# Optimization experiments

Hardware: AMD Instinct MI355X
Metric: run time of the kernel (lower is better)

The kernel has to match this reference:

```python
import jax, jax.numpy as jnp
import numpy as np

DIM = 4096
HID = DIM // 4
CAPACITY = 0.5
TEMPERATURE = 1.0


def setup_inputs() -> dict:
    key = jax.random.key(0)
    k_x, k_w1, k_w2 = jax.random.split(key, 3)
    B, S = 4, 4096
    x = jax.random.normal(k_x, (B, S, DIM), dtype=jnp.float32)
    # Linear params (kaiming-ish scale)
    w1 = jax.random.normal(k_w1, (DIM, HID), dtype=jnp.float32) * (1.0 / np.sqrt(DIM))
    b1 = jnp.zeros((HID,), dtype=jnp.float32)
    w2 = jax.random.normal(k_w2, (HID, 1), dtype=jnp.float32) * (1.0 / np.sqrt(HID))
    b2 = jnp.zeros((1,), dtype=jnp.float32)
    return {"x": x, "w1": w1, "b1": b1, "w2": w2, "b2": b2}


def reference(x, w1, b1, w2, b2):
    B, S, _ = x.shape
    # tiny MLP scorer: dim -> dim//4 -> 1
    h = jax.nn.relu(jnp.einsum('bsd,dh->bsh', x, w1) + b1)
    scores = (jnp.einsum('bsh,ho->bso', h, w2) + b2)[..., 0] / TEMPERATURE  # [B, S]
    k = int(S * CAPACITY)
    topk_scores, topk_idx = jax.lax.top_k(scores, k)  # [B, k]
    rows = jnp.arange(B)[:, None]
    mask = jnp.zeros((B, S), dtype=jnp.bool_).at[rows, topk_idx].set(True)
    # torch: routing_weights[mask] = softmax(topk_scores).flatten()
    # mask-indexed assignment writes to positions in ascending index order,
    # while values stay in topk (descending-score) order -> replicate exactly.
    sorted_idx = jnp.sort(topk_idx, axis=-1)  # [B, k], ascending positions
    soft = jax.nn.softmax(topk_scores, axis=-1)  # [B, k], topk order
    routing_weights = jnp.zeros((B, S), dtype=scores.dtype).at[rows, sorted_idx].set(soft)
    return mask, routing_weights
```

## Files before the change

### kernel.cpp

```cpp
#include <hip/hip_runtime.h>
#include <math.h>

typedef _Float16 f16;
typedef _Float16 f16x8 __attribute__((ext_vector_type(8)));
typedef float    f32x4 __attribute__((ext_vector_type(4)));

#define DIMK 4096
#define HIDN 1024
#define NTOK 16384
#define SLEN 4096
#define NBATCH 4
#define KSEL 2048
#define NPART 16

#define LO_SCALE 2048.0f
#define INV_ACC_SCALE (1.0f/4194304.0f)

__device__ __forceinline__ void load_lds16(const void* g, void* l) {
    __builtin_amdgcn_global_load_lds(
        (const __attribute__((address_space(1))) unsigned int*)g,
        (__attribute__((address_space(3))) unsigned int*)l, 16, 0, 0);
}
__device__ __forceinline__ int swzf(int row) { return ((row >> 1) & 3) << 4; }

__device__ __forceinline__ void split_w(float v, f16& hi_s, f16& lo_s) {
    const f16 h = (f16)v;
    const float hf = (float)h;
    hi_s = (f16)(hf * LO_SCALE);
    lo_s = (f16)((v - hf) * LO_SCALE);
}

__device__ __forceinline__ void split8(const float4 v0, const float4 v1,
                                       f16x8& h8, f16x8& l8) {
    const float s0 = v0.x * LO_SCALE, s1 = v0.y * LO_SCALE;
    const float s2 = v0.z * LO_SCALE, s3 = v0.w * LO_SCALE;
    const float s4 = v1.x * LO_SCALE, s5 = v1.y * LO_SCALE;
    const float s6 = v1.z * LO_SCALE, s7 = v1.w * LO_SCALE;
    const auto h01 = __builtin_amdgcn_cvt_pkrtz(s0, s1);
    const auto h23 = __builtin_amdgcn_cvt_pkrtz(s2, s3);
    const auto h45 = __builtin_amdgcn_cvt_pkrtz(s4, s5);
    const auto h67 = __builtin_amdgcn_cvt_pkrtz(s6, s7);
    const auto l01 = __builtin_amdgcn_cvt_pkrtz(s0 - (float)h01[0], s1 - (float)h01[1]);
    const auto l23 = __builtin_amdgcn_cvt_pkrtz(s2 - (float)h23[0], s3 - (float)h23[1]);
    const auto l45 = __builtin_amdgcn_cvt_pkrtz(s4 - (float)h45[0], s5 - (float)h45[1]);
    const auto l67 = __builtin_amdgcn_cvt_pkrtz(s6 - (float)h67[0], s7 - (float)h67[1]);
    h8 = f16x8{(f16)h01[0], (f16)h01[1], (f16)h23[0], (f16)h23[1],
               (f16)h45[0], (f16)h45[1], (f16)h67[0], (f16)h67[1]};
    l8 = f16x8{(f16)l01[0], (f16)l01[1], (f16)l23[0], (f16)l23[1],
               (f16)l45[0], (f16)l45[1], (f16)l67[0], (f16)l67[1]};
}

__device__ __forceinline__ f32x4 mfma16(f16x8 a, f16x8 b, f32x4 c) {
    return __builtin_amdgcn_mfma_f32_16x16x32_f16(a, b, c, 0, 0, 0);
}

__global__ __launch_bounds__(256) void conv_w1_kernel(
    const float* w1, f16* wthi, f16* wtlo)
{
    __shared__ float t[64][65];
    const int bx = blockIdx.x & 15;
    const int by = blockIdx.x >> 4;
    #pragma unroll
    for (int i = 0; i < 16; ++i) {
        const int e = threadIdx.x + i * 256;
        const int r = e >> 6, c = e & 63;
        t[r][c] = w1[(size_t)(by * 64 + r) * HIDN + bx * 64 + c];
    }
    __syncthreads();
    #pragma unroll
    for (int i = 0; i < 16; ++i) {
        const int e = threadIdx.x + i * 256;
        const int nrow = e >> 6, kcol = e & 63;
        f16 h, l;
        split_w(t[kcol][nrow], h, l);
        const size_t o = (size_t)(bx * 64 + nrow) * DIMK + by * 64 + kcol;
        wthi[o] = h;
        wtlo[o] = l;
    }
}

#define TBM 256
#define TBN 256
#define TBK 32
#define BUF_BYTES 65536

__global__ __launch_bounds__(512, 2) void mod_mfma256_kernel(
    const float* x, const f16* wthi, const f16* wtlo,
    const float* b1, const float* w2, float* partials)
{
    __shared__ __align__(16) char lds[2 * BUF_BYTES];

    const int tid  = threadIdx.x;
    const int lane = tid & 63;
    const int wid  = tid >> 6;
    const int wr   = wid >> 2;
    const int wc   = wid & 3;

    const int bid  = blockIdx.x;
    const int v    = (bid & 7) * 32 + (bid >> 3);
    const int nblk = v & 3;
    const int mblk = v >> 2;
    const int tokBase = mblk * TBM;
    const int nBase   = nblk * TBN;

    int arow[2], akqq[2], adst[2];
    #pragma unroll
    for (int i = 0; i < 2; ++i) {
        const int p = tid + i * 512;
        arow[i] = p >> 2;
        akqq[i] = p & 3;
        adst[i] = arow[i] * 64 + ((akqq[i] ^ ((arow[i] >> 1) & 3)) << 4);
    }
    const f16* bsrcm[4];
    int bsrcoff[4], bdst[4];
    #pragma unroll
    for (int j = 0; j < 4; ++j) {
        const int c    = wid * 4 + j;
        const int half = c >> 4;
        const int rloc = (c & 15) * 16 + (lane >> 2);
        bsrcm[j]   = half ? wtlo : wthi;
        bsrcoff[j] = (nBase + rloc) * (DIMK * 2) + (((lane & 3) << 4) ^ swzf(rloc));
        bdst[j]    = 32768 + half * 16384 + (c & 15) * 1024;
    }

    int aoff[8], boff[4];
    #pragma unroll
    for (int m = 0; m < 8; ++m) {
        const int r = wr * 128 + m * 16 + (lane & 15);
        aoff[m] = r * 64 + (((lane >> 4) ^ ((r >> 1) & 3)) << 4);
    }
    #pragma unroll
    for (int n = 0; n < 4; ++n) {
        const int c = wc * 64 + n * 16 + (lane & 15);
        boff[n] = 32768 + c * 64 + (((lane >> 4) ^ ((c >> 1) & 3)) << 4);
    }

    f32x4 acc[8][4];
    #pragma unroll
    for (int m = 0; m < 8; ++m)
        #pragma unroll
        for (int n = 0; n < 4; ++n)
            #pragma unroll
            for (int j = 0; j < 4; ++j) acc[m][n][j] = 0.0f;

    {
        float4 a0[2], a1[2];
        #pragma unroll
        for (int i = 0; i < 2; ++i) {
            const float* src = x + (size_t)(tokBase + arow[i]) * DIMK + akqq[i] * 8;
            a0[i] = *(const float4*)(src);
            a1[i] = *(const float4*)(src + 4);
        }
        #pragma unroll
        for (int j = 0; j < 4; ++j)
            load_lds16((const char*)bsrcm[j] + bsrcoff[j], lds + bdst[j]);
        #pragma unroll
        for (int i = 0; i < 2; ++i) {
            f16x8 h8, l8;
            split8(a0[i], a1[i], h8, l8);
            *(f16x8*)(lds + adst[i]) = h8;
            *(f16x8*)(lds + 16384 + adst[i]) = l8;
        }
        __syncthreads();
    }

    for (int t = 0; t < DIMK / TBK; ++t) {
        const int cur = (t & 1) * BUF_BYTES;
        const int nxt = BUF_BYTES - cur;
        const bool pf = (t + 1 < DIMK / TBK);
        const int k0n = (t + 1) * TBK;

        float4 a0[2], a1[2];
        if (pf) {
            #pragma unroll
            for (int i = 0; i < 2; ++i) {
                const float* src = x + (size_t)(tokBase + arow[i]) * DIMK + k0n + akqq[i] * 8;
                a0[i] = *(const float4*)(src);
                a1[i] = *(const float4*)(src + 4);
            }
            #pragma unroll
            for (int j = 0; j < 4; ++j)
                load_lds16((const char*)bsrcm[j] + bsrcoff[j] + k0n * 2, lds + nxt + bdst[j]);
        }

        f16x8 afh[4], afl[4], bh0[2], bl0[2], bh1[2], bl1[2];
        #pragma unroll
        for (int m = 0; m < 4; ++m) {
            afh[m] = *(const f16x8*)(lds + cur + aoff[m]);
            afl[m] = *(const f16x8*)(lds + cur + 16384 + aoff[m]);
        }
        #pragma unroll
        for (int n = 0; n < 2; ++n) {
            bh0[n] = *(const f16x8*)(lds + cur + boff[n]);
            bl0[n] = *(const f16x8*)(lds + cur + 16384 + boff[n]);
        }
        __builtin_amdgcn_s_setprio(1);
        #pragma unroll
        for (int m = 0; m < 4; ++m)
            #pragma unroll
            for (int n = 0; n < 2; ++n) {
                acc[m][n] = mfma16(afh[m], bh0[n], acc[m][n]);
                acc[m][n] = mfma16(afh[m], bl0[n], acc[m][n]);
                acc[m][n] = mfma16(afl[m], bh0[n], acc[m][n]);
            }
        __builtin_amdgcn_s_setprio(0);
        #pragma unroll
        for (int n = 0; n < 2; ++n) {
            bh1[n] = *(const f16x8*)(lds + cur + boff[2 + n]);
            bl1[n] = *(const f16x8*)(lds + cur + 16384 + boff[2 + n]);
        }
        __builtin_amdgcn_s_setprio(1);
        #pragma unroll
        for (int m = 0; m < 4; ++m)
            #pragma unroll
            for (int n = 0; n < 2; ++n) {
                acc[m][2 + n] = mfma16(afh[m], bh1[n], acc[m][2 + n]);
                acc[m][2 + n] = mfma16(afh[m], bl1[n], acc[m][2 + n]);
                acc[m][2 + n] = mfma16(afl[m], bh1[n], acc[m][2 + n]);
            }
        __builtin_amdgcn_s_setprio(0);
        if (pf) {
            #pragma unroll
            for (int i = 0; i < 2; ++i) {
                f16x8 h8, l8;
                split8(a0[i], a1[i], h8, l8);
                *(f16x8*)(lds + nxt + adst[i]) = h8;
                *(f16x8*)(lds + nxt + 16384 + adst[i]) = l8;
            }
        }
        #pragma unroll
        for (int m = 0; m < 4; ++m) {
            afh[m] = *(const f16x8*)(lds + cur + aoff[4 + m]);
            afl[m] = *(const f16x8*)(lds + cur + 16384 + aoff[4 + m]);
        }
        __builtin_amdgcn_s_setprio(1);
        #pragma unroll
        for (int m = 0; m < 4; ++m)
            #pragma unroll
            for (int n = 0; n < 2; ++n) {
                acc[4 + m][n] = mfma16(afh[m], bh0[n], acc[4 + m][n]);
                acc[4 + m][n] = mfma16(afh[m], bl0[n], acc[4 + m][n]);
                acc[4 + m][n] = mfma16(afl[m], bh0[n], acc[4 + m][n]);
            }
        __builtin_amdgcn_s_setprio(0);
        __builtin_amdgcn_s_setprio(1);
        #pragma unroll
        for (int m = 0; m < 4; ++m)
            #pragma unroll
            for (int n = 0; n < 2; ++n) {
                acc[4 + m][2 + n] = mfma16(afh[m], bh1[n], acc[4 + m][2 + n]);
                acc[4 + m][2 + n] = mfma16(afh[m], bl1[n], acc[4 + m][2 + n]);
                acc[4 + m][2 + n] = mfma16(afl[m], bh1[n], acc[4 + m][2 + n]);
            }
        __builtin_amdgcn_s_setprio(0);

        __syncthreads();
    }

    float rp[8][4];
    #pragma unroll
    for (int m = 0; m < 8; ++m)
        #pragma unroll
        for (int j = 0; j < 4; ++j) rp[m][j] = 0.0f;

    #pragma unroll
    for (int n = 0; n < 4; ++n) {
        const int col = nBase + wc * 64 + n * 16 + (lane & 15);
        const float wv = w2[col];
        const float bb = b1[col];
        #pragma unroll
        for (int m = 0; m < 8; ++m)
            #pragma unroll
            for (int j = 0; j < 4; ++j) {
                float h = fmaf(acc[m][n][j], INV_ACC_SCALE, bb);
                h = fmaxf(h, 0.0f);
                rp[m][j] = fmaf(h, wv, rp[m][j]);
            }
    }
    #pragma unroll
    for (int off = 1; off < 16; off <<= 1)
        #pragma unroll
        for (int m = 0; m < 8; ++m)
            #pragma unroll
            for (int j = 0; j < 4; ++j)
                rp[m][j] += __shfl_xor(rp[m][j], off, 64);

    if ((lane & 15) == 0) {
        const int q = lane >> 4;
        const int slot = nblk * 4 + wc;
        float* pdst = partials + (size_t)slot * NTOK + tokBase + wr * 128 + q * 4;
        #pragma unroll
        for (int m = 0; m < 8; ++m)
            #pragma unroll
            for (int j = 0; j < 4; ++j)
                pdst[m * 16 + j] = rp[m][j];
    }
}

__global__ __launch_bounds__(1024) void mod_route_part_kernel(
    const float* partials, const float* b2,
    float* mask_out, float* rw_out)
{
    __shared__ float s[SLEN];
    __shared__ int   sg[2][1024];
    __shared__ int   se[2][1024];
    __shared__ float red[1024];

    const int b   = blockIdx.x;
    const int tid = threadIdx.x;
    const int base = tid * 4;
    const float bias2 = b2[0];

    float og[4];
    #pragma unroll
    for (int u = 0; u < 4; ++u) {
        const size_t tok = (size_t)b * SLEN + base + u;
        float sum = bias2;
        #pragma unroll
        for (int p = 0; p < NPART; ++p) sum += partials[(size_t)p * NTOK + tok];
        og[u] = sum;
        s[base + u] = sum;
    }
    __syncthreads();

    for (int k = 2; k <= SLEN; k <<= 1) {
        for (int j = k >> 1; j > 0; j >>= 1) {
            for (int i = tid; i < SLEN; i += 1024) {
                const int ixj = i ^ j;
                if (ixj > i) {
                    const float a = s[i];
                    const float c = s[ixj];
                    const bool descRegion = ((i & k) == 0);
                    if (descRegion ? (a < c) : (a > c)) { s[i] = c; s[ixj] = a; }
                }
            }
            __syncthreads();
        }
    }

    const float maxv      = s[0];
    const float threshold = s[KSEL - 1];

    float part = 0.f;
    for (int i = tid; i < KSEL; i += 1024) part += expf(s[i] - maxv);
    red[tid] = part;
    __syncthreads();
    for (int off = 512; off > 0; off >>= 1) {
        if (tid < off) red[tid] += red[tid + off];
        __syncthreads();
    }
    const float sumexp = red[0];
    __syncthreads();

    int gcnt = 0, ecnt = 0;
    #pragma unroll
    for (int u = 0; u < 4; ++u) {
        gcnt += (og[u] > threshold);
        ecnt += (og[u] == threshold);
    }

    int cur = 0;
    sg[0][tid] = gcnt;
    se[0][tid] = ecnt;
    __syncthreads();
    for (int off = 1; off < 1024; off <<= 1) {
        const int nxt = cur ^ 1;
        int vg = sg[cur][tid];
        int ve = se[cur][tid];
        if (tid >= off) { vg += sg[cur][tid - off]; ve += se[cur][tid - off]; }
        sg[nxt][tid] = vg;
        se[nxt][tid] = ve;
        __syncthreads();
        cur = nxt;
    }
    const int total_gt = sg[cur][1023];
    const int R = KSEL - total_gt;
    int pgi = sg[cur][tid] - gcnt;
    int pei = se[cur][tid] - ecnt;

    const float inv_sum = 1.0f / sumexp;
    #pragma unroll
    for (int u = 0; u < 4; ++u) {
        const bool isg = og[u] > threshold;
        const bool ise = og[u] == threshold;
        const bool sel = isg || (ise && pei < R);
        float rwv = 0.f;
        if (sel) {
            const int rank = pgi + (pei < R ? pei : R);
            rwv = expf(s[rank] - maxv) * inv_sum;
        }
        const size_t oi = (size_t)b * SLEN + base + u;
        mask_out[oi] = sel ? 1.0f : 0.0f;
        rw_out[oi]   = rwv;
        pgi += isg;
        pei += ise;
    }
}

#define BM 64
#define BN 256
#define BK 32
#define THREADS 512

__global__ __launch_bounds__(THREADS) void mod_score_kernel(
    const float* x, const float* w1, const float* b1,
    const float* w2, const float* b2, float* scores)
{
    __shared__ float Xs[BK][BM + 4];
    __shared__ float Ws[BK][BN];

    const int tid = threadIdx.x;
    const int tx = tid & 31;
    const int ty = tid >> 5;
    const int tokBase = blockIdx.x * BM;

    float sp[4] = {0.f, 0.f, 0.f, 0.f};
    const float bias2 = b2[0];

    for (int hc = 0; hc < HIDN; hc += BN) {
        float acc[4][8];
        #pragma unroll
        for (int m = 0; m < 4; ++m)
            #pragma unroll
            for (int n = 0; n < 8; ++n) acc[m][n] = 0.f;

        for (int k0 = 0; k0 < DIMK; k0 += BK) {
            {
                const int r  = tid >> 3;
                const int c4 = tid & 7;
                const float4 vv = *(const float4*)(x + (size_t)(tokBase + r) * DIMK + k0 + c4 * 4);
                Xs[c4 * 4 + 0][r] = vv.x;
                Xs[c4 * 4 + 1][r] = vv.y;
                Xs[c4 * 4 + 2][r] = vv.z;
                Xs[c4 * 4 + 3][r] = vv.w;
            }
            #pragma unroll
            for (int i = 0; i < 4; ++i) {
                const int idx = tid + i * THREADS;
                const int r   = idx >> 6;
                const int c4  = idx & 63;
                const float4 vv = *(const float4*)(w1 + (size_t)(k0 + r) * HIDN + hc + c4 * 4);
                *(float4*)&Ws[r][c4 * 4] = vv;
            }
            __syncthreads();

            #pragma unroll 8
            for (int k = 0; k < BK; ++k) {
                const float4 xv = *(const float4*)&Xs[k][ty * 4];
                const float4 wa = *(const float4*)&Ws[k][tx * 4];
                const float4 wb = *(const float4*)&Ws[k][128 + tx * 4];
                const float xm[4] = {xv.x, xv.y, xv.z, xv.w};
                const float wn[8] = {wa.x, wa.y, wa.z, wa.w, wb.x, wb.y, wb.z, wb.w};
                #pragma unroll
                for (int m = 0; m < 4; ++m)
                    #pragma unroll
                    for (int n = 0; n < 8; ++n)
                        acc[m][n] = fmaf(xm[m], wn[n], acc[m][n]);
            }
            __syncthreads();
        }

        #pragma unroll
        for (int half = 0; half < 2; ++half) {
            #pragma unroll
            for (int n = 0; n < 4; ++n) {
                const int h = hc + half * 128 + tx * 4 + n;
                const float wv = w2[h];
                const float bb = b1[h];
                #pragma unroll
                for (int m = 0; m < 4; ++m) {
                    float hv = acc[m][half * 4 + n] + bb;
                    hv = fmaxf(hv, 0.f);
                    sp[m] = fmaf(hv, wv, sp[m]);
                }
            }
        }
    }

    #pragma unroll
    for (int off = 1; off < 32; off <<= 1) {
        #pragma unroll
        for (int m = 0; m < 4; ++m) sp[m] += __shfl_xor(sp[m], off, 64);
    }
    if (tx == 0) {
        #pragma unroll
        for (int m = 0; m < 4; ++m)
            scores[tokBase + ty * 4 + m] = sp[m] + bias2;
    }
}

__global__ __launch_bounds__(1024) void mod_route_kernel(
    const float* scores, float* mask_out, float* rw_out)
{
    __shared__ float s[SLEN];
    __shared__ int   sg[2][1024];
    __shared__ int   se[2][1024];
    __shared__ float red[1024];

    const int b   = blockIdx.x;
    const int tid = threadIdx.x;
    const float* rowp = scores + (size_t)b * SLEN;
    const int base = tid * 4;

    const float4 ov = *(const float4*)(rowp + base);
    float og[4] = {ov.x, ov.y, ov.z, ov.w};
    s[base + 0] = ov.x;
    s[base + 1] = ov.y;
    s[base + 2] = ov.z;
    s[base + 3] = ov.w;
    __syncthreads();

    for (int k = 2; k <= SLEN; k <<= 1) {
        for (int j = k >> 1; j > 0; j >>= 1) {
            for (int i = tid; i < SLEN; i += 1024) {
                const int ixj = i ^ j;
                if (ixj > i) {
                    const float a = s[i];
                    const float c = s[ixj];
                    const bool descRegion = ((i & k) == 0);
                    if (descRegion ? (a < c) : (a > c)) { s[i] = c; s[ixj] = a; }
                }
            }
            __syncthreads();
        }
    }

    const float maxv      = s[0];
    const float threshold = s[KSEL - 1];

    float part = 0.f;
    for (int i = tid; i < KSEL; i += 1024) part += expf(s[i] - maxv);
    red[tid] = part;
    __syncthreads();
    for (int off = 512; off > 0; off >>= 1) {
        if (tid < off) red[tid] += red[tid + off];
        __syncthreads();
    }
    const float sumexp = red[0];
    __syncthreads();

    int gcnt = 0, ecnt = 0;
    #pragma unroll
    for (int u = 0; u < 4; ++u) {
        gcnt += (og[u] > threshold);
        ecnt += (og[u] == threshold);
    }

    int cur = 0;
    sg[0][tid] = gcnt;
    se[0][tid] = ecnt;
    __syncthreads();
    for (int off = 1; off < 1024; off <<= 1) {
        const int nxt = cur ^ 1;
        int vg = sg[cur][tid];
        int ve = se[cur][tid];
        if (tid >= off) { vg += sg[cur][tid - off]; ve += se[cur][tid - off]; }
        sg[nxt][tid] = vg;
        se[nxt][tid] = ve;
        __syncthreads();
        cur = nxt;
    }
    const int total_gt = sg[cur][1023];
    const int R = KSEL - total_gt;
    int pgi = sg[cur][tid] - gcnt;
    int pei = se[cur][tid] - ecnt;

    const float inv_sum = 1.0f / sumexp;
    #pragma unroll
    for (int u = 0; u < 4; ++u) {
        const bool isg = og[u] > threshold;
        const bool ise = og[u] == threshold;
        const bool sel = isg || (ise && pei < R);
        float rwv = 0.f;
        if (sel) {
            const int rank = pgi + (pei < R ? pei : R);
            rwv = expf(s[rank] - maxv) * inv_sum;
        }
        const size_t oi = (size_t)b * SLEN + base + u;
        mask_out[oi] = sel ? 1.0f : 0.0f;
        rw_out[oi]   = rwv;
        pgi += isg;
        pei += ise;
    }
}

extern "C" void kernel_launch(void* const* d_in, const int* in_sizes, int n_in,
                              void* d_out, int out_size, void* d_ws, size_t ws_size,
                              hipStream_t stream) {
    const float* x  = (const float*)d_in[0];
    const float* w1 = (const float*)d_in[1];
    const float* b1 = (const float*)d_in[2];
    const float* w2 = (const float*)d_in[3];
    const float* b2 = (const float*)d_in[4];

    float* out      = (float*)d_out;
    float* mask_out = out;
    float* rw_out   = out + NTOK;

    const size_t partials_b = (size_t)NPART * NTOK * 4;
    const size_t wsplit_b   = (size_t)HIDN * DIMK * 2;
    const size_t needed     = partials_b + 2 * wsplit_b;

    if (ws_size >= needed) {
        char* wsb = (char*)d_ws;
        float* partials = (float*)wsb;
        f16* wthi = (f16*)(wsb + partials_b);
        f16* wtlo = wthi + (size_t)HIDN * DIMK;

        conv_w1_kernel<<<1024, 256, 0, stream>>>(w1, wthi, wtlo);
        mod_mfma256_kernel<<<256, 512, 0, stream>>>(x, wthi, wtlo, b1, w2, partials);
        mod_route_part_kernel<<<NBATCH, 1024, 0, stream>>>(partials, b2, mask_out, rw_out);
    } else {
        float* scores = (ws_size >= (size_t)NTOK * sizeof(float)) ? (float*)d_ws : rw_out;
        mod_score_kernel<<<NTOK / BM, THREADS, 0, stream>>>(x, w1, b1, w2, b2, scores);
        mod_route_kernel<<<NBATCH, 1024, 0, stream>>>(scores, mask_out, rw_out);
    }
}
```

Measured before the change: 399.1 us.

## Double GEMM block to 1024 threads with 64x64 per-wave tiles

Raises the fused scorer GEMM block from 512 to 1024 threads (16 waves), halving each wave's output tile from 128x64 to 64x64. Each thread now stages one A row chunk and two B chunks per K step. The MFMA inner loop is reorganised into three passes (hi*hi, hi*lo, lo*hi), reloading B hi fragments. The aim is more waves per CU to hide latency, at the cost of less register-level reuse per wave, more LDS fragment reads per MFMA, and register pressure from the tighter launch bounds.

```diff
diff --git a/kernel.cpp b/kernel.cpp
--- a/kernel.cpp
+++ b/kernel.cpp
@@ -84,7 +84,7 @@
 #define TBK 32
 #define BUF_BYTES 65536
 
-__global__ __launch_bounds__(512, 2) void mod_mfma256_kernel(
+__global__ __launch_bounds__(1024, 4) void mod_mfma256_kernel(
     const float* x, const f16* wthi, const f16* wtlo,
     const float* b1, const float* w2, float* partials)
 {
@@ -103,19 +103,15 @@
     const int tokBase = mblk * TBM;
     const int nBase   = nblk * TBN;
 
-    int arow[2], akqq[2], adst[2];
-    #pragma unroll
-    for (int i = 0; i < 2; ++i) {
-        const int p = tid + i * 512;
-        arow[i] = p >> 2;
-        akqq[i] = p & 3;
-        adst[i] = arow[i] * 64 + ((akqq[i] ^ ((arow[i] >> 1) & 3)) << 4);
-    }
-    const f16* bsrcm[4];
-    int bsrcoff[4], bdst[4];
-    #pragma unroll
-    for (int j = 0; j < 4; ++j) {
-        const int c    = wid * 4 + j;
+    const int arow = tid >> 2;
+    const int akq  = tid & 3;
+    const int adst = arow * 64 + ((akq ^ ((arow >> 1) & 3)) << 4);
+
+    const f16* bsrcm[2];
+    int bsrcoff[2], bdst[2];
+    #pragma unroll
+    for (int j = 0; j < 2; ++j) {
+        const int c    = wid * 2 + j;
         const int half = c >> 4;
         const int rloc = (c & 15) * 16 + (lane >> 2);
         bsrcm[j]   = half ? wtlo : wthi;
@@ -123,10 +119,10 @@
         bdst[j]    = 32768 + half * 16384 + (c & 15) * 1024;
     }
 
-    int aoff[8], boff[4];
-    #pragma unroll
-    for (int m = 0; m < 8; ++m) {
-        const int r = wr * 128 + m * 16 + (lane & 15);
+    int aoff[4], boff[4];
+    #pragma unroll
+    for (int m = 0; m < 4; ++m) {
+        const int r = wr * 64 + m * 16 + (lane & 15);
         aoff[m] = r * 64 + (((lane >> 4) ^ ((r >> 1) & 3)) << 4);
     }
     #pragma unroll
@@ -135,32 +131,25 @@
         boff[n] = 32768 + c * 64 + (((lane >> 4) ^ ((c >> 1) & 3)) << 4);
     }
 
-    f32x4 acc[8][4];
-    #pragma unroll
-    for (int m = 0; m < 8; ++m)
+    f32x4 acc[4][4];
+    #pragma unroll
+    for (int m = 0; m < 4; ++m)
         #pragma unroll
         for (int n = 0; n < 4; ++n)
             #pragma unroll
             for (int j = 0; j < 4; ++j) acc[m][n][j] = 0.0f;
 
     {
-        float4 a0[2], a1[2];
-        #pragma unroll
-        for (int i = 0; i < 2; ++i) {
-            const float* src = x + (size_t)(tokBase + arow[i]) * DIMK + akqq[i] * 8;
-            a0[i] = *(const float4*)(src);
-            a1[i] = *(const float4*)(src + 4);
-        }
-        #pragma unroll
-        for (int j = 0; j < 4; ++j)
+        const float* src = x + (size_t)(tokBase + arow) * DIMK + akq * 8;
+        const float4 a0 = *(const float4*)(src);
+        const float4 a1 = *(const float4*)(src + 4);
+        #pragma unroll
+        for (int j = 0; j < 2; ++j)
             load_lds16((const char*)bsrcm[j] + bsrcoff[j], lds + bdst[j]);
-        #pragma unroll
-        for (int i = 0; i < 2; ++i) {
-            f16x8 h8, l8;
-            split8(a0[i], a1[i], h8, l8);
-            *(f16x8*)(lds + adst[i]) = h8;
-            *(f16x8*)(lds + 16384 + adst[i]) = l8;
-        }
+        f16x8 h8, l8;
+        split8(a0, a1, h8, l8);
+        *(f16x8*)(lds + adst) = h8;
+        *(f16x8*)(lds + 16384 + adst) = l8;
         __syncthreads();
     }
 
@@ -170,96 +159,69 @@
         const bool pf = (t + 1 < DIMK / TBK);
         const int k0n = (t + 1) * TBK;
 
-        float4 a0[2], a1[2];
+        float4 a0, a1;
         if (pf) {
-            #pragma unroll
-            for (int i = 0; i < 2; ++i) {
-                const float* src = x + (size_t)(tokBase + arow[i]) * DIMK + k0n + akqq[i] * 8;
-                a0[i] = *(const float4*)(src);
-                a1[i] = *(const float4*)(src + 4);
-            }
-            #pragma unroll
-            for (int j = 0; j < 4; ++j)
+            const float* src = x + (size_t)(tokBase + arow) * DIMK + k0n + akq * 8;
+            a0 = *(const float4*)(src);
+            a1 = *(const float4*)(src + 4);
+            #pragma unroll
+            for (int j = 0; j < 2; ++j)
                 load_lds16((const char*)bsrcm[j] + bsrcoff[j] + k0n * 2, lds + nxt + bdst[j]);
         }
 
-        f16x8 afh[4], afl[4], bh0[2], bl0[2], bh1[2], bl1[2];
-        #pragma unroll
-        for (int m = 0; m < 4; ++m) {
-            afh[m] = *(const f16x8*)(lds + cur + aoff[m]);
-            afl[m] = *(const f16x8*)(lds + cur + 16384 + aoff[m]);
-        }
-        #pragma unroll
-        for (int n = 0; n < 2; ++n) {
-            bh0[n] = *(const f16x8*)(lds + cur + boff[n]);
-            bl0[n] = *(const f16x8*)(lds + cur + 16384 + boff[n]);
-        }
+        f16x8 fa[4], fb[4];
+        #pragma unroll
+        for (int m = 0; m < 4; ++m)
+            fa[m] = *(const f16x8*)(lds + cur + aoff[m]);
+        #pragma unroll
+        for (int n = 0; n < 4; ++n)
+            fb[n] = *(const f16x8*)(lds + cur + boff[n]);
         __builtin_amdgcn_s_setprio(1);
         #pragma unroll
         for (int m = 0; m < 4; ++m)
             #pragma unroll
-            for (int n = 0; n < 2; ++n) {
-                acc[m][n] = mfma16(afh[m], bh0[n], acc[m][n]);
-                acc[m][n] = mfma16(afh[m], bl0[n], acc[m][n]);
-                acc[m][n] = mfma16(afl[m], bh0[n], acc[m][n]);
-            }
+            for (int n = 0; n < 4; ++n)
+                acc[m][n] = mfma16(fa[m], fb[n], acc[m][n]);
         __builtin_amdgcn_s_setprio(0);
-        #pragma unroll
-        for (int n = 0; n < 2; ++n) {
-            bh1[n] = *(const f16x8*)(lds + cur + boff[2 + n]);
-            bl1[n] = *(const f16x8*)(lds + cur + 16384 + boff[2 + n]);
-        }
+
+        #pragma unroll
+        for (int n = 0; n < 4; ++n)
+            fb[n] = *(const f16x8*)(lds + cur + 16384 + boff[n]);
         __builtin_amdgcn_s_setprio(1);
         #pragma unroll
         for (int m = 0; m < 4; ++m)
             #pragma unroll
-            for (int n = 0; n < 2; ++n) {
-                acc[m][2 + n] = mfma16(afh[m], bh1[n], acc[m][2 + n]);
-                acc[m][2 + n] = mfma16(afh[m], bl1[n], acc[m][2 + n]);
-                acc[m][2 + n] = mfma16(afl[m], bh1[n], acc[m][2 + n]);
-            }
+            for (int n = 0; n < 4; ++n)
+                acc[m][n] = mfma16(fa[m], fb[n], acc[m][n]);
         __builtin_amdgcn_s_setprio(0);
+
         if (pf) {
-            #pragma unroll
-            for (int i = 0; i < 2; ++i) {
-                f16x8 h8, l8;
-                split8(a0[i], a1[i], h8, l8);
-                *(f16x8*)(lds + nxt + adst[i]) = h8;
-                *(f16x8*)(lds + nxt + 16384 + adst[i]) = l8;
-            }
-        }
-        #pragma unroll
-        for (int m = 0; m < 4; ++m) {
-            afh[m] = *(const f16x8*)(lds + cur + aoff[4 + m]);
-            afl[m] = *(const f16x8*)(lds + cur + 16384 + aoff[4 + m]);
-        }
+            f16x8 h8, l8;
+            split8(a0, a1, h8, l8);
+            *(f16x8*)(lds + nxt + adst) = h8;
+            *(f16x8*)(lds + nxt + 16384 + adst) = l8;
+        }
+
+        #pragma unroll
+        for (int m = 0; m < 4; ++m)
+            fa[m] = *(const f16x8*)(lds + cur + 16384 + aoff[m]);
+        #pragma unroll
+        for (int n = 0; n < 4; ++n)
+            fb[n] = *(const f16x8*)(lds + cur + boff[n]);
         __builtin_amdgcn_s_setprio(1);
         #pragma unroll
         for (int m = 0; m < 4; ++m)
             #pragma unroll
-            for (int n = 0; n < 2; ++n) {
-                acc[4 + m][n] = mfma16(afh[m], bh0[n], acc[4 + m][n]);
-                acc[4 + m][n] = mfma16(afh[m], bl0[n], acc[4 + m][n]);
-                acc[4 + m][n] = mfma16(afl[m], bh0[n], acc[4 + m][n]);
-            }
+            for (int n = 0; n < 4; ++n)
+                acc[m][n] = mfma16(fa[m], fb[n], acc[m][n]);
         __builtin_amdgcn_s_setprio(0);
-        __builtin_amdgcn_s_setprio(1);
-        #pragma unroll
-        for (int m = 0; m < 4; ++m)
-            #pragma unroll
-            for (int n = 0; n < 2; ++n) {
-                acc[4 + m][2 + n] = mfma16(afh[m], bh1[n], acc[4 + m][2 + n]);
-                acc[4 + m][2 + n] = mfma16(afh[m], bl1[n], acc[4 + m][2 + n]);
-                acc[4 + m][2 + n] = mfma16(afl[m], bh1[n], acc[4 + m][2 + n]);
-            }
-        __builtin_amdgcn_s_setprio(0);
 
         __syncthreads();
     }
 
-    float rp[8][4];
-    #pragma unroll
-    for (int m = 0; m < 8; ++m)
+    float rp[4][4];
+    #pragma unroll
+    for (int m = 0; m < 4; ++m)
         #pragma unroll
         for (int j = 0; j < 4; ++j) rp[m][j] = 0.0f;
 
@@ -269,7 +231,7 @@
         const float wv = w2[col];
         const float bb = b1[col];
         #pragma unroll
-        for (int m = 0; m < 8; ++m)
+        for (int m = 0; m < 4; ++m)
             #pragma unroll
             for (int j = 0; j < 4; ++j) {
                 float h = fmaf(acc[m][n][j], INV_ACC_SCALE, bb);
@@ -280,7 +242,7 @@
     #pragma unroll
     for (int off = 1; off < 16; off <<= 1)
         #pragma unroll
-        for (int m = 0; m < 8; ++m)
+        for (int m = 0; m < 4; ++m)
             #pragma unroll
             for (int j = 0; j < 4; ++j)
                 rp[m][j] += __shfl_xor(rp[m][j], off, 64);
@@ -288,9 +250,9 @@
     if ((lane & 15) == 0) {
         const int q = lane >> 4;
         const int slot = nblk * 4 + wc;
-        float* pdst = partials + (size_t)slot * NTOK + tokBase + wr * 128 + q * 4;
-        #pragma unroll
-        for (int m = 0; m < 8; ++m)
+        float* pdst = partials + (size_t)slot * NTOK + tokBase + wr * 64 + q * 4;
+        #pragma unroll
+        for (int m = 0; m < 4; ++m)
             #pragma unroll
             for (int j = 0; j < 4; ++j)
                 pdst[m * 16 + j] = rp[m][j];
@@ -608,7 +570,7 @@
         f16* wtlo = wthi + (size_t)HIDN * DIMK;
 
         conv_w1_kernel<<<1024, 256, 0, stream>>>(w1, wthi, wtlo);
-        mod_mfma256_kernel<<<256, 512, 0, stream>>>(x, wthi, wtlo, b1, w2, partials);
+        mod_mfma256_kernel<<<256, 1024, 0, stream>>>(x, wthi, wtlo, b1, w2, partials);
         mod_route_part_kernel<<<NBATCH, 1024, 0, stream>>>(partials, b2, mask_out, rw_out);
     } else {
         float* scores = (ws_size >= (size_t)NTOK * sizeof(float)) ? (float*)d_ws : rw_out;
```

New measurement: 401.7 us, median of 2. No clear change (+0.6%).

## Restructure GEMM main loop into barrier-interleaved phases with split prefetch

Applied to the files above, without the earlier changes.

Reorganizes the split-fp16 GEMM inner loop into two halves of three MFMA phases each, separated by workgroup barriers in a ping-pong style schedule. Global loads of x and the LDS-direct loads of w1 are spread across the phases instead of being issued together at the top. Fragment registers are reduced by reloading the B fragments per phase. The explicit __syncthreads is replaced by raw s_barrier plus a manual vmcnt wait, which adds barrier overhead and risks ordering hazards on LDS writes if the waits are not sufficient.

```diff
diff --git a/kernel.cpp b/kernel.cpp
--- a/kernel.cpp
+++ b/kernel.cpp
@@ -171,90 +171,88 @@
         const int k0n = (t + 1) * TBK;
 
         float4 a0[2], a1[2];
-        if (pf) {
-            #pragma unroll
-            for (int i = 0; i < 2; ++i) {
-                const float* src = x + (size_t)(tokBase + arow[i]) * DIMK + k0n + akqq[i] * 8;
-                a0[i] = *(const float4*)(src);
-                a1[i] = *(const float4*)(src + 4);
-            }
-            #pragma unroll
-            for (int j = 0; j < 4; ++j)
-                load_lds16((const char*)bsrcm[j] + bsrcoff[j] + k0n * 2, lds + nxt + bdst[j]);
-        }
-
-        f16x8 afh[4], afl[4], bh0[2], bl0[2], bh1[2], bl1[2];
-        #pragma unroll
-        for (int m = 0; m < 4; ++m) {
-            afh[m] = *(const f16x8*)(lds + cur + aoff[m]);
-            afl[m] = *(const f16x8*)(lds + cur + 16384 + aoff[m]);
-        }
-        #pragma unroll
-        for (int n = 0; n < 2; ++n) {
-            bh0[n] = *(const f16x8*)(lds + cur + boff[n]);
-            bl0[n] = *(const f16x8*)(lds + cur + 16384 + boff[n]);
-        }
-        __builtin_amdgcn_s_setprio(1);
-        #pragma unroll
-        for (int m = 0; m < 4; ++m)
-            #pragma unroll
-            for (int n = 0; n < 2; ++n) {
-                acc[m][n] = mfma16(afh[m], bh0[n], acc[m][n]);
-                acc[m][n] = mfma16(afh[m], bl0[n], acc[m][n]);
-                acc[m][n] = mfma16(afl[m], bh0[n], acc[m][n]);
-            }
-        __builtin_amdgcn_s_setprio(0);
-        #pragma unroll
-        for (int n = 0; n < 2; ++n) {
-            bh1[n] = *(const f16x8*)(lds + cur + boff[2 + n]);
-            bl1[n] = *(const f16x8*)(lds + cur + 16384 + boff[2 + n]);
-        }
-        __builtin_amdgcn_s_setprio(1);
-        #pragma unroll
-        for (int m = 0; m < 4; ++m)
-            #pragma unroll
-            for (int n = 0; n < 2; ++n) {
-                acc[m][2 + n] = mfma16(afh[m], bh1[n], acc[m][2 + n]);
-                acc[m][2 + n] = mfma16(afh[m], bl1[n], acc[m][2 + n]);
-                acc[m][2 + n] = mfma16(afl[m], bh1[n], acc[m][2 + n]);
-            }
-        __builtin_amdgcn_s_setprio(0);
-        if (pf) {
-            #pragma unroll
-            for (int i = 0; i < 2; ++i) {
-                f16x8 h8, l8;
-                split8(a0[i], a1[i], h8, l8);
-                *(f16x8*)(lds + nxt + adst[i]) = h8;
-                *(f16x8*)(lds + nxt + 16384 + adst[i]) = l8;
-            }
-        }
-        #pragma unroll
-        for (int m = 0; m < 4; ++m) {
-            afh[m] = *(const f16x8*)(lds + cur + aoff[4 + m]);
-            afl[m] = *(const f16x8*)(lds + cur + 16384 + aoff[4 + m]);
-        }
-        __builtin_amdgcn_s_setprio(1);
-        #pragma unroll
-        for (int m = 0; m < 4; ++m)
-            #pragma unroll
-            for (int n = 0; n < 2; ++n) {
-                acc[4 + m][n] = mfma16(afh[m], bh0[n], acc[4 + m][n]);
-                acc[4 + m][n] = mfma16(afh[m], bl0[n], acc[4 + m][n]);
-                acc[4 + m][n] = mfma16(afl[m], bh0[n], acc[4 + m][n]);
-            }
-        __builtin_amdgcn_s_setprio(0);
-        __builtin_amdgcn_s_setprio(1);
-        #pragma unroll
-        for (int m = 0; m < 4; ++m)
-            #pragma unroll
-            for (int n = 0; n < 2; ++n) {
-                acc[4 + m][2 + n] = mfma16(afh[m], bh1[n], acc[4 + m][2 + n]);
-                acc[4 + m][2 + n] = mfma16(afh[m], bl1[n], acc[4 + m][2 + n]);
-                acc[4 + m][2 + n] = mfma16(afl[m], bh1[n], acc[4 + m][2 + n]);
-            }
-        __builtin_amdgcn_s_setprio(0);
-
-        __syncthreads();
+        f16x8 fa[4], fb[4];
+
+        #pragma unroll
+        for (int h = 0; h < 2; ++h) {
+            const int hs = h * 4;
+
+            #pragma unroll
+            for (int m = 0; m < 4; ++m)
+                fa[m] = *(const f16x8*)(lds + cur + aoff[hs + m]);
+            #pragma unroll
+            for (int n = 0; n < 4; ++n)
+                fb[n] = *(const f16x8*)(lds + cur + boff[n]);
+            if (h == 0) {
+                if (pf) {
+                    #pragma unroll
+                    for (int i = 0; i < 2; ++i) {
+                        const float* src = x + (size_t)(tokBase + arow[i]) * DIMK + k0n + akqq[i] * 8;
+                        a0[i] = *(const float4*)(src);
+                        a1[i] = *(const float4*)(src + 4);
+                    }
+                }
+            } else {
+                if (pf) {
+                    #pragma unroll
+                    for (int i = 0; i < 2; ++i) {
+                        f16x8 h8, l8;
+                        split8(a0[i], a1[i], h8, l8);
+                        *(f16x8*)(lds + nxt + adst[i]) = h8;
+                        *(f16x8*)(lds + nxt + 16384 + adst[i]) = l8;
+                    }
+                }
+            }
+            __builtin_amdgcn_s_barrier();
+            __builtin_amdgcn_s_setprio(1);
+            #pragma unroll
+            for (int m = 0; m < 4; ++m)
+                #pragma unroll
+                for (int n = 0; n < 4; ++n)
+                    acc[hs + m][n] = mfma16(fa[m], fb[n], acc[hs + m][n]);
+            __builtin_amdgcn_s_setprio(0);
+            __builtin_amdgcn_s_barrier();
+
+            #pragma unroll
+            for (int n = 0; n < 4; ++n)
+                fb[n] = *(const f16x8*)(lds + cur + 16384 + boff[n]);
+            if (pf) {
+                #pragma unroll
+                for (int j = 0; j < 2; ++j) {
+                    const int jj = h * 2 + j;
+                    load_lds16((const char*)bsrcm[jj] + bsrcoff[jj] + k0n * 2,
+                               lds + nxt + bdst[jj]);
+                }
+            }
+            __builtin_amdgcn_s_barrier();
+            __builtin_amdgcn_s_setprio(1);
+            #pragma unroll
+            for (int m = 0; m < 4; ++m)
+                #pragma unroll
+                for (int n = 0; n < 4; ++n)
+                    acc[hs + m][n] = mfma16(fa[m], fb[n], acc[hs + m][n]);
+            __builtin_amdgcn_s_setprio(0);
+            __builtin_amdgcn_s_barrier();
+
+            #pragma unroll
+            for (int m = 0; m < 4; ++m)
+                fa[m] = *(const f16x8*)(lds + cur + 16384 + aoff[hs + m]);
+            #pragma unroll
+            for (int n = 0; n < 4; ++n)
+                fb[n] = *(const f16x8*)(lds + cur + boff[n]);
+            __builtin_amdgcn_s_barrier();
+            __builtin_amdgcn_s_setprio(1);
+            #pragma unroll
+            for (int m = 0; m < 4; ++m)
+                #pragma unroll
+                for (int n = 0; n < 4; ++n)
+                    acc[hs + m][n] = mfma16(fa[m], fb[n], acc[hs + m][n]);
+            __builtin_amdgcn_s_setprio(0);
+            if (h == 1) {
+                asm volatile("s_waitcnt vmcnt(0)" ::: "memory");
+            }
+            __builtin_amdgcn_s_barrier();
+        }
     }
 
     float rp[8][4];
```

After: 417.7 us. 4.6% more time.
